# Kernel tuning notes

Hardware: AMD Instinct MI355X
Metric: run time of the kernel (lower is better)

## Reference

```python
import jax, jax.numpy as jnp
import numpy as np

B, S, H, HKV, D = 2, 1024, 32, 8, 128


def _rope_tables(seq_len, head_dim, base=10000.0):
    inv_freq = 1.0 / (base ** (np.arange(0, head_dim, 2, dtype=np.float32) / head_dim))
    freqs = np.arange(seq_len, dtype=np.float32)[:, None] * inv_freq[None, :]  # [S, D/2]
    emb = np.concatenate([freqs, freqs], axis=-1)  # [S, D] (Llama layout)
    return jnp.asarray(np.cos(emb)), jnp.asarray(np.sin(emb))


def setup_inputs() -> dict:
    key = jax.random.key(0)
    kq, kk, kv = jax.random.split(key, 3)
    q = jax.random.normal(kq, (B, S, H, D), dtype=jnp.float32)
    k = jax.random.normal(kk, (B, S, HKV, D), dtype=jnp.float32)
    v = jax.random.normal(kv, (B, S, HKV, D), dtype=jnp.float32)
    cos, sin = _rope_tables(S, D)
    # additive causal mask [B, 1, S, S]: 0 where allowed, large negative where masked
    causal = jnp.tril(jnp.ones((S, S), dtype=bool))
    mask = jnp.where(causal, 0.0, -1e9).astype(jnp.float32)
    attention_mask = jnp.broadcast_to(mask[None, None], (B, 1, S, S))
    softmax_scale = 1.0 / float(np.sqrt(D))
    return {
        "query_states": q, "key_states": k, "value_states": v,
        "cos": cos, "sin": sin, "attention_mask": attention_mask,
        "softmax_scale": softmax_scale,
    }


def _apply_rope(x, cos, sin):
    # x: [B, S, h, D]; cos/sin: [S, D]
    d2 = x.shape[-1] // 2
    rot = jnp.concatenate([-x[..., d2:], x[..., :d2]], axis=-1)  # rotate_half
    return x * cos[None, :, None, :] + rot * sin[None, :, None, :]


def reference(query_states, key_states, value_states, cos, sin, attention_mask, softmax_scale):
    b, s, h, d = query_states.shape
    hkv = key_states.shape[2]
    g = h // hkv  # GQA group size
    q = _apply_rope(query_states, cos, sin)
    k = _apply_rope(key_states, cos, sin)
    qg = q.reshape(b, s, hkv, g, d)
    # scores: [B, Hkv, G, Q, K]
    scores = jnp.einsum('bqhgd,bkhd->bhgqk', qg, k) * softmax_scale
    scores = scores + attention_mask[:, :, None]  # [B,1,Q,K] -> broadcast over (Hkv, G)
    p = jax.nn.softmax(scores, axis=-1)
    out = jnp.einsum('bhgqk,bkhd->bqhgd', p, value_states)
    return out.reshape(b, s, h, d)
```

## Files before the change

### kernel.cpp

```cpp
#include <hip/hip_runtime.h>

#define S_LEN 1024
#define D_DIM 128
#define NH    32
#define NKV   8
#define NB    2

typedef __bf16 bf16x8 __attribute__((ext_vector_type(8)));
typedef float  f32x16 __attribute__((ext_vector_type(16)));
typedef unsigned short u16x8 __attribute__((ext_vector_type(8)));
typedef unsigned int   u32x4 __attribute__((ext_vector_type(4)));

__device__ __forceinline__ unsigned short f2bf(float f) {
    unsigned int u = __float_as_uint(f);
    u += 0x7fffu + ((u >> 16) & 1u);
    return (unsigned short)(u >> 16);
}

__device__ __forceinline__ void gld_lds16(const unsigned short* g, unsigned short* l) {
    __builtin_amdgcn_global_load_lds(
        (const __attribute__((address_space(1))) unsigned int*)(g),
        (__attribute__((address_space(3))) unsigned int*)(l), 16, 0, 0);
}

__global__ __launch_bounds__(256) void prep_kernel(
    const float* __restrict__ q, const float* __restrict__ k,
    const float* __restrict__ v, const float* __restrict__ cosb,
    const float* __restrict__ sinb, const float* __restrict__ scale_ptr,
    unsigned short* __restrict__ Qr, unsigned short* __restrict__ Kr,
    unsigned short* __restrict__ Vt)
{
    const int bx  = blockIdx.x;
    const int tid = threadIdx.x;
    __shared__ __align__(16) unsigned short tile[64][132];
    if (bx < 16384) {
        const float sc = *scale_ptr * 1.44269504088896f;
        int gid = bx * 256 + tid;
        int row = gid >> 6;
        int j   = gid & 63;
        int h  = row & (NH - 1);
        int bs = row >> 5;
        int s  = bs & (S_LEN - 1);
        int b  = bs >> 10;
        const float* qp = q + (size_t)row * D_DIM;
        float x0 = qp[j];
        float x1 = qp[j + 64];
        float c  = cosb[s * D_DIM + j];
        float sn = sinb[s * D_DIM + j];
        size_t orow = ((size_t)(b * NH + h) * S_LEN + s) * D_DIM;
        Qr[orow + j]      = f2bf((x0 * c - x1 * sn) * sc);
        Qr[orow + j + 64] = f2bf((x1 * c + x0 * sn) * sc);
    } else if (bx < 20480) {
        int gid = (bx - 16384) * 256 + tid;
        int row = gid >> 6;
        int j   = gid & 63;
        int hk = row & (NKV - 1);
        int bs = row >> 3;
        int s  = bs & (S_LEN - 1);
        int b  = bs >> 10;
        const float* kp = k + (size_t)row * D_DIM;
        float x0 = kp[j];
        float x1 = kp[j + 64];
        float c  = cosb[s * D_DIM + j];
        float sn = sinb[s * D_DIM + j];
        size_t orow = ((size_t)(b * NKV + hk) * S_LEN + s) * D_DIM;
        Kr[orow + j]      = f2bf(x0 * c - x1 * sn);
        Kr[orow + j + 64] = f2bf(x1 * c + x0 * sn);
    } else {
        int blk   = bx - 20480;
        int stile = blk & 15;
        int hk    = (blk >> 4) & (NKV - 1);
        int b     = blk >> 7;
#pragma unroll
        for (int i = 0; i < 8; i++) {
            int e    = i * 256 + tid;
            int srow = e >> 5;
            int dq   = (e & 31) * 4;
            const float* vp = v + (((size_t)(b * S_LEN + stile * 64 + srow) * NKV + hk) * D_DIM + dq);
            float4 val = *(const float4*)vp;
            tile[srow][dq + 0] = f2bf(val.x);
            tile[srow][dq + 1] = f2bf(val.y);
            tile[srow][dq + 2] = f2bf(val.z);
            tile[srow][dq + 3] = f2bf(val.w);
        }
        __syncthreads();
        size_t head = (size_t)(b * NKV + hk) * D_DIM * S_LEN;
#pragma unroll
        for (int i = 0; i < 4; i++) {
            int g  = i * 256 + tid;
            int d  = g >> 3;
            int c8 = g & 7;
            int s0 = c8 * 8;
            u16x8 pk;
#pragma unroll
            for (int jj = 0; jj < 8; jj++) pk[jj] = tile[s0 + jj][d];
            *(u16x8*)(Vt + head + (size_t)d * S_LEN + stile * 64 + s0) = pk;
        }
    }
}

__global__ __launch_bounds__(256) void attn_kernel(
    const unsigned short* __restrict__ Qr,
    const unsigned short* __restrict__ Kr,
    const unsigned short* __restrict__ Vt,
    float* __restrict__ out)
{
    const int bid  = blockIdx.x;
    const int qt   = 7 - (bid >> 6);
    const int head = bid & 63;
    const int h    = head & 31;
    const int b    = head >> 5;
    const int hk   = h >> 2;

    const int tid  = threadIdx.x;
    const int w    = tid >> 6;
    const int lane = tid & 63;
    const int ln   = lane & 31;
    const int hi   = lane >> 5;

    __shared__ __align__(16) unsigned short Kt[2][64 * 128];
    __shared__ __align__(16) unsigned short Vs[2][128 * 64];

    const int q0 = qt * 128 + w * 32;
    const int qg = q0 + ln;
    const int U  = 2 * qt + 2;

    const unsigned short* khead = Kr + (size_t)(b * NKV + hk) * S_LEN * D_DIM;
    const unsigned short* vhead = Vt + (size_t)(b * NKV + hk) * D_DIM * S_LEN;

    const int krow = lane >> 4;
    const int kcc  = lane & 15;
    const int vrw  = lane >> 3;
    const int vcc  = lane & 7;

    auto stage = [&](int u, int buf) {
        const unsigned short* kt = khead + (size_t)u * 64 * D_DIM;
#pragma unroll
        for (int n = 0; n < 4; n++) {
            int row = w * 16 + n * 4 + krow;
            int cc  = kcc ^ (row & 7);
            gld_lds16(kt + (size_t)row * D_DIM + cc * 8, &Kt[buf][(w * 16 + n * 4) * 128]);
        }
        const unsigned short* vt = vhead + (size_t)u * 64;
#pragma unroll
        for (int n = 0; n < 4; n++) {
            int d  = w * 32 + n * 8 + vrw;
            int cc = vcc ^ (d & 7);
            gld_lds16(vt + (size_t)d * S_LEN + cc * 8, &Vs[buf][(w * 32 + n * 8) * 64]);
        }
    };

    const unsigned short* qrow =
        Qr + ((size_t)(b * NH + h) * S_LEN + qg) * D_DIM + hi * 8;
    bf16x8 qf[8];
#pragma unroll
    for (int dd = 0; dd < 8; dd++)
        qf[dd] = *(const bf16x8*)(qrow + dd * 16);

    f32x16 o[4];
#pragma unroll
    for (int dt = 0; dt < 4; dt++)
#pragma unroll
        for (int r = 0; r < 16; r++) o[dt][r] = 0.f;
    float m_run = -1e30f, lsum = 0.f;

    stage(0, 0);

#pragma unroll 1
    for (int u = 0; u < U; ++u) {
        const int cur = u & 1;
        __syncthreads();
        if (u + 1 < U) stage(u + 1, cur ^ 1);

        if (64 * u <= q0 + 31) {
            const bool act1 = (64 * u + 32 <= q0 + 31);

            f32x16 st[2];
#pragma unroll
            for (int r = 0; r < 16; r++) { st[0][r] = 0.f; st[1][r] = 0.f; }
            __builtin_amdgcn_s_setprio(1);
#pragma unroll
            for (int s = 0; s < 2; s++) {
                if (s == 0 || act1) {
#pragma unroll
                    for (int dd = 0; dd < 8; dd++) {
                        int row = s * 32 + ln;
                        int c   = (2 * dd + hi) ^ (row & 7);
                        bf16x8 kf = *(const bf16x8*)(&Kt[cur][row * 128 + c * 8]);
                        st[s] = __builtin_amdgcn_mfma_f32_32x32x16_bf16(kf, qf[dd], st[s], 0, 0, 0);
                    }
                }
            }
            __builtin_amdgcn_s_setprio(0);

            if (64 * u + 63 > q0) {
#pragma unroll
                for (int s = 0; s < 2; s++)
#pragma unroll
                    for (int r = 0; r < 16; r++) {
                        int kg = 64 * u + 32 * s + (r & 3) + 8 * (r >> 2) + 4 * hi;
                        if (kg > qg) st[s][r] = -1e30f;
                    }
            }

            float mx = -1e30f;
#pragma unroll
            for (int r = 0; r < 16; r++) mx = fmaxf(mx, st[0][r]);
            if (act1) {
#pragma unroll
                for (int r = 0; r < 16; r++) mx = fmaxf(mx, st[1][r]);
            }
            float pm = fmaxf(mx, __shfl_xor(mx, 32));

            if (__any(pm > m_run + 8.f)) {
                float mnew = fmaxf(m_run, pm);
                float ps   = exp2f(m_run - mnew);
                m_run = mnew;
                lsum *= ps;
#pragma unroll
                for (int r = 0; r < 16; r++) {
                    float psr = __shfl(ps, (r & 3) + 8 * (r >> 2) + 4 * hi);
#pragma unroll
                    for (int dt = 0; dt < 4; dt++) o[dt][r] *= psr;
                }
            }
            float ls = 0.f;
#pragma unroll
            for (int r = 0; r < 16; r++) {
                float p = exp2f(st[0][r] - m_run);
                st[0][r] = p; ls += p;
            }
            if (act1) {
#pragma unroll
                for (int r = 0; r < 16; r++) {
                    float p = exp2f(st[1][r] - m_run);
                    st[1][r] = p; ls += p;
                }
            }
            lsum += ls + __shfl_xor(ls, 32);

            const char* vbase = (const char*)&Vs[cur][0];
            __builtin_amdgcn_s_setprio(1);
#pragma unroll
            for (int ks = 0; ks < 4; ks++) {
                if (ks < 2 || act1) {
                    const f32x16& sv = st[ks >> 1];
                    const int g = (ks & 1) * 8;
                    unsigned int d0 = (unsigned)f2bf(sv[g + 0]) | ((unsigned)f2bf(sv[g + 1]) << 16);
                    unsigned int d1 = (unsigned)f2bf(sv[g + 2]) | ((unsigned)f2bf(sv[g + 3]) << 16);
                    unsigned int d2 = (unsigned)f2bf(sv[g + 4]) | ((unsigned)f2bf(sv[g + 5]) << 16);
                    unsigned int d3 = (unsigned)f2bf(sv[g + 6]) | ((unsigned)f2bf(sv[g + 7]) << 16);
                    u32x4 paw = {d0, d1, d2, d3};
                    bf16x8 pa = __builtin_bit_cast(bf16x8, paw);
#pragma unroll
                    for (int dt = 0; dt < 4; dt++) {
                        int d = dt * 32 + ln;
                        const char* vrow = vbase + d * 128;
                        int x = d & 7;
                        uint2 vlo = *(const uint2*)(vrow + (((2 * ks)     ^ x) * 16) + hi * 8);
                        uint2 vhi = *(const uint2*)(vrow + (((2 * ks + 1) ^ x) * 16) + hi * 8);
                        u32x4 vw = {vlo.x, vlo.y, vhi.x, vhi.y};
                        bf16x8 vf = __builtin_bit_cast(bf16x8, vw);
                        o[dt] = __builtin_amdgcn_mfma_f32_32x32x16_bf16(pa, vf, o[dt], 0, 0, 0);
                    }
                }
            }
            __builtin_amdgcn_s_setprio(0);
        }
    }

    float rcp = 1.0f / lsum;
    float* ob = out + ((size_t)(b * S_LEN + q0) * NH + h) * D_DIM;
#pragma unroll
    for (int r = 0; r < 16; r++) {
        int qo = (r & 3) + 8 * (r >> 2) + 4 * hi;
        float invr = __shfl(rcp, qo);
#pragma unroll
        for (int dt = 0; dt < 4; dt++)
            ob[(size_t)qo * NH * D_DIM + dt * 32 + ln] = o[dt][r] * invr;
    }
}

extern "C" void kernel_launch(void* const* d_in, const int* in_sizes, int n_in,
                              void* d_out, int out_size, void* d_ws, size_t ws_size,
                              hipStream_t stream) {
    const float* q    = (const float*)d_in[0];
    const float* k    = (const float*)d_in[1];
    const float* v    = (const float*)d_in[2];
    const float* cosb = (const float*)d_in[3];
    const float* sinb = (const float*)d_in[4];
    const float* scale = (const float*)d_in[6];
    float* out = (float*)d_out;

    unsigned short* Qr = (unsigned short*)d_ws;
    unsigned short* Kr = Qr + (size_t)NB * NH  * S_LEN * D_DIM;
    unsigned short* Vt = Kr + (size_t)NB * NKV * S_LEN * D_DIM;

    prep_kernel<<<20736, 256, 0, stream>>>(q, k, v, cosb, sinb, scale, Qr, Kr, Vt);
    attn_kernel<<<512, 256, 0, stream>>>(Qr, Kr, Vt, out);
}
```

Baseline: 75.92 us.

## Use single-wave attention blocks reading K/V directly from global memory

Replaces the 4-wave workgroup, which staged K and V tiles into LDS with double-buffered async loads, with one-wave workgroups of 32 query rows. Each wave reads K and V straight from global memory through the caches, and a new block-index mapping interleaves heads and balances causal work by pairing long and short query tiles. This removes LDS staging and block barriers and gives the scheduler more independent waves. In exchange, the K/V reuse that LDS provided across the four waves is lost, so more global and L2 traffic is needed, and the V loads become scattered 8-byte reads.

```diff
diff --git a/kernel.cpp b/kernel.cpp
--- a/kernel.cpp
+++ b/kernel.cpp
@@ -15,12 +15,6 @@
     unsigned int u = __float_as_uint(f);
     u += 0x7fffu + ((u >> 16) & 1u);
     return (unsigned short)(u >> 16);
-}
-
-__device__ __forceinline__ void gld_lds16(const unsigned short* g, unsigned short* l) {
-    __builtin_amdgcn_global_load_lds(
-        (const __attribute__((address_space(1))) unsigned int*)(g),
-        (__attribute__((address_space(3))) unsigned int*)(l), 16, 0, 0);
 }
 
 __global__ __launch_bounds__(256) void prep_kernel(
@@ -99,56 +93,35 @@
     }
 }
 
-__global__ __launch_bounds__(256) void attn_kernel(
+__global__ __launch_bounds__(64) void attn_kernel(
     const unsigned short* __restrict__ Qr,
     const unsigned short* __restrict__ Kr,
     const unsigned short* __restrict__ Vt,
     float* __restrict__ out)
 {
-    const int bid  = blockIdx.x;
-    const int qt   = 7 - (bid >> 6);
-    const int head = bid & 63;
-    const int h    = head & 31;
-    const int b    = head >> 5;
-    const int hk   = h >> 2;
-
-    const int tid  = threadIdx.x;
-    const int w    = tid >> 6;
-    const int lane = tid & 63;
+    const int bid = blockIdx.x;
+    const int c   = bid & 255;
+    const int s   = bid >> 8;
+    const int sj  = s & 3;
+    const int hl  = s >> 2;
+    const int cc  = c >> 6;
+    const int m16 = 4 * cc + sj;
+    const int qt  = hl ? (2 * m16) : (31 - 2 * m16);
+    const int head = (c & 7) + 8 * ((c >> 3) & 7);
+    const int h   = head & 31;
+    const int b   = head >> 5;
+    const int hk  = h >> 2;
+
+    const int lane = threadIdx.x;
     const int ln   = lane & 31;
     const int hi   = lane >> 5;
 
-    __shared__ __align__(16) unsigned short Kt[2][64 * 128];
-    __shared__ __align__(16) unsigned short Vs[2][128 * 64];
-
-    const int q0 = qt * 128 + w * 32;
+    const int q0 = qt * 32;
     const int qg = q0 + ln;
-    const int U  = 2 * qt + 2;
+    const int U  = (qt >> 1) + 1;
 
     const unsigned short* khead = Kr + (size_t)(b * NKV + hk) * S_LEN * D_DIM;
     const unsigned short* vhead = Vt + (size_t)(b * NKV + hk) * D_DIM * S_LEN;
-
-    const int krow = lane >> 4;
-    const int kcc  = lane & 15;
-    const int vrw  = lane >> 3;
-    const int vcc  = lane & 7;
-
-    auto stage = [&](int u, int buf) {
-        const unsigned short* kt = khead + (size_t)u * 64 * D_DIM;
-#pragma unroll
-        for (int n = 0; n < 4; n++) {
-            int row = w * 16 + n * 4 + krow;
-            int cc  = kcc ^ (row & 7);
-            gld_lds16(kt + (size_t)row * D_DIM + cc * 8, &Kt[buf][(w * 16 + n * 4) * 128]);
-        }
-        const unsigned short* vt = vhead + (size_t)u * 64;
-#pragma unroll
-        for (int n = 0; n < 4; n++) {
-            int d  = w * 32 + n * 8 + vrw;
-            int cc = vcc ^ (d & 7);
-            gld_lds16(vt + (size_t)d * S_LEN + cc * 8, &Vs[buf][(w * 32 + n * 8) * 64]);
-        }
-    };
 
     const unsigned short* qrow =
         Qr + ((size_t)(b * NH + h) * S_LEN + qg) * D_DIM + hi * 8;
@@ -164,109 +137,99 @@
         for (int r = 0; r < 16; r++) o[dt][r] = 0.f;
     float m_run = -1e30f, lsum = 0.f;
 
-    stage(0, 0);
-
 #pragma unroll 1
     for (int u = 0; u < U; ++u) {
-        const int cur = u & 1;
-        __syncthreads();
-        if (u + 1 < U) stage(u + 1, cur ^ 1);
-
-        if (64 * u <= q0 + 31) {
-            const bool act1 = (64 * u + 32 <= q0 + 31);
-
-            f32x16 st[2];
-#pragma unroll
-            for (int r = 0; r < 16; r++) { st[0][r] = 0.f; st[1][r] = 0.f; }
-            __builtin_amdgcn_s_setprio(1);
-#pragma unroll
-            for (int s = 0; s < 2; s++) {
-                if (s == 0 || act1) {
-#pragma unroll
-                    for (int dd = 0; dd < 8; dd++) {
-                        int row = s * 32 + ln;
-                        int c   = (2 * dd + hi) ^ (row & 7);
-                        bf16x8 kf = *(const bf16x8*)(&Kt[cur][row * 128 + c * 8]);
-                        st[s] = __builtin_amdgcn_mfma_f32_32x32x16_bf16(kf, qf[dd], st[s], 0, 0, 0);
-                    }
+        const unsigned short* kt = khead + (size_t)u * 64 * D_DIM;
+        const unsigned short* vt = vhead + u * 64;
+        const bool act1 = (64 * u + 32 <= q0 + 31);
+
+        f32x16 st[2];
+#pragma unroll
+        for (int r = 0; r < 16; r++) { st[0][r] = 0.f; st[1][r] = 0.f; }
+        __builtin_amdgcn_s_setprio(1);
+#pragma unroll
+        for (int s2 = 0; s2 < 2; s2++) {
+            if (s2 == 0 || act1) {
+                const unsigned short* krow = kt + (size_t)(s2 * 32 + ln) * D_DIM + hi * 8;
+#pragma unroll
+                for (int dd = 0; dd < 8; dd++) {
+                    bf16x8 kf = *(const bf16x8*)(krow + dd * 16);
+                    st[s2] = __builtin_amdgcn_mfma_f32_32x32x16_bf16(kf, qf[dd], st[s2], 0, 0, 0);
                 }
             }
-            __builtin_amdgcn_s_setprio(0);
-
-            if (64 * u + 63 > q0) {
-#pragma unroll
-                for (int s = 0; s < 2; s++)
-#pragma unroll
-                    for (int r = 0; r < 16; r++) {
-                        int kg = 64 * u + 32 * s + (r & 3) + 8 * (r >> 2) + 4 * hi;
-                        if (kg > qg) st[s][r] = -1e30f;
-                    }
-            }
-
-            float mx = -1e30f;
-#pragma unroll
-            for (int r = 0; r < 16; r++) mx = fmaxf(mx, st[0][r]);
-            if (act1) {
-#pragma unroll
-                for (int r = 0; r < 16; r++) mx = fmaxf(mx, st[1][r]);
-            }
-            float pm = fmaxf(mx, __shfl_xor(mx, 32));
-
-            if (__any(pm > m_run + 8.f)) {
-                float mnew = fmaxf(m_run, pm);
-                float ps   = exp2f(m_run - mnew);
-                m_run = mnew;
-                lsum *= ps;
+        }
+        __builtin_amdgcn_s_setprio(0);
+
+        if (64 * u + 63 > q0) {
+#pragma unroll
+            for (int s2 = 0; s2 < 2; s2++)
 #pragma unroll
                 for (int r = 0; r < 16; r++) {
-                    float psr = __shfl(ps, (r & 3) + 8 * (r >> 2) + 4 * hi);
-#pragma unroll
-                    for (int dt = 0; dt < 4; dt++) o[dt][r] *= psr;
+                    int kg = 64 * u + 32 * s2 + (r & 3) + 8 * (r >> 2) + 4 * hi;
+                    if (kg > qg) st[s2][r] = -1e30f;
                 }
-            }
-            float ls = 0.f;
+        }
+
+        float mx = -1e30f;
+#pragma unroll
+        for (int r = 0; r < 16; r++) mx = fmaxf(mx, st[0][r]);
+        if (act1) {
+#pragma unroll
+            for (int r = 0; r < 16; r++) mx = fmaxf(mx, st[1][r]);
+        }
+        float pm = fmaxf(mx, __shfl_xor(mx, 32));
+
+        if (__any(pm > m_run + 8.f)) {
+            float mnew = fmaxf(m_run, pm);
+            float ps   = exp2f(m_run - mnew);
+            m_run = mnew;
+            lsum *= ps;
 #pragma unroll
             for (int r = 0; r < 16; r++) {
-                float p = exp2f(st[0][r] - m_run);
-                st[0][r] = p; ls += p;
-            }
-            if (act1) {
-#pragma unroll
-                for (int r = 0; r < 16; r++) {
-                    float p = exp2f(st[1][r] - m_run);
-                    st[1][r] = p; ls += p;
+                float psr = __shfl(ps, (r & 3) + 8 * (r >> 2) + 4 * hi);
+#pragma unroll
+                for (int dt = 0; dt < 4; dt++) o[dt][r] *= psr;
+            }
+        }
+        float ls = 0.f;
+#pragma unroll
+        for (int r = 0; r < 16; r++) {
+            float p = exp2f(st[0][r] - m_run);
+            st[0][r] = p; ls += p;
+        }
+        if (act1) {
+#pragma unroll
+            for (int r = 0; r < 16; r++) {
+                float p = exp2f(st[1][r] - m_run);
+                st[1][r] = p; ls += p;
+            }
+        }
+        lsum += ls + __shfl_xor(ls, 32);
+
+        __builtin_amdgcn_s_setprio(1);
+#pragma unroll
+        for (int ks = 0; ks < 4; ks++) {
+            if (ks < 2 || act1) {
+                const f32x16& sv = st[ks >> 1];
+                const int g = (ks & 1) * 8;
+                unsigned int d0 = (unsigned)f2bf(sv[g + 0]) | ((unsigned)f2bf(sv[g + 1]) << 16);
+                unsigned int d1 = (unsigned)f2bf(sv[g + 2]) | ((unsigned)f2bf(sv[g + 3]) << 16);
+                unsigned int d2 = (unsigned)f2bf(sv[g + 4]) | ((unsigned)f2bf(sv[g + 5]) << 16);
+                unsigned int d3 = (unsigned)f2bf(sv[g + 6]) | ((unsigned)f2bf(sv[g + 7]) << 16);
+                u32x4 paw = {d0, d1, d2, d3};
+                bf16x8 pa = __builtin_bit_cast(bf16x8, paw);
+#pragma unroll
+                for (int dt = 0; dt < 4; dt++) {
+                    const unsigned short* vrow = vt + (size_t)(dt * 32 + ln) * S_LEN;
+                    uint2 vlo = *(const uint2*)(vrow + ks * 16 + hi * 4);
+                    uint2 vhi2 = *(const uint2*)(vrow + ks * 16 + 8 + hi * 4);
+                    u32x4 vw = {vlo.x, vlo.y, vhi2.x, vhi2.y};
+                    bf16x8 vf = __builtin_bit_cast(bf16x8, vw);
+                    o[dt] = __builtin_amdgcn_mfma_f32_32x32x16_bf16(pa, vf, o[dt], 0, 0, 0);
                 }
             }
-            lsum += ls + __shfl_xor(ls, 32);
-
-            const char* vbase = (const char*)&Vs[cur][0];
-            __builtin_amdgcn_s_setprio(1);
-#pragma unroll
-            for (int ks = 0; ks < 4; ks++) {
-                if (ks < 2 || act1) {
-                    const f32x16& sv = st[ks >> 1];
-                    const int g = (ks & 1) * 8;
-                    unsigned int d0 = (unsigned)f2bf(sv[g + 0]) | ((unsigned)f2bf(sv[g + 1]) << 16);
-                    unsigned int d1 = (unsigned)f2bf(sv[g + 2]) | ((unsigned)f2bf(sv[g + 3]) << 16);
-                    unsigned int d2 = (unsigned)f2bf(sv[g + 4]) | ((unsigned)f2bf(sv[g + 5]) << 16);
-                    unsigned int d3 = (unsigned)f2bf(sv[g + 6]) | ((unsigned)f2bf(sv[g + 7]) << 16);
-                    u32x4 paw = {d0, d1, d2, d3};
-                    bf16x8 pa = __builtin_bit_cast(bf16x8, paw);
-#pragma unroll
-                    for (int dt = 0; dt < 4; dt++) {
-                        int d = dt * 32 + ln;
-                        const char* vrow = vbase + d * 128;
-                        int x = d & 7;
-                        uint2 vlo = *(const uint2*)(vrow + (((2 * ks)     ^ x) * 16) + hi * 8);
-                        uint2 vhi = *(const uint2*)(vrow + (((2 * ks + 1) ^ x) * 16) + hi * 8);
-                        u32x4 vw = {vlo.x, vlo.y, vhi.x, vhi.y};
-                        bf16x8 vf = __builtin_bit_cast(bf16x8, vw);
-                        o[dt] = __builtin_amdgcn_mfma_f32_32x32x16_bf16(pa, vf, o[dt], 0, 0, 0);
-                    }
-                }
-            }
-            __builtin_amdgcn_s_setprio(0);
-        }
+        }
+        __builtin_amdgcn_s_setprio(0);
     }
 
     float rcp = 1.0f / lsum;
@@ -297,5 +260,5 @@
     unsigned short* Vt = Kr + (size_t)NB * NKV * S_LEN * D_DIM;
 
     prep_kernel<<<20736, 256, 0, stream>>>(q, k, v, cosb, sinb, scale, Qr, Kr, Vt);
-    attn_kernel<<<512, 256, 0, stream>>>(Qr, Kr, Vt, out);
-}
+    attn_kernel<<<2048, 64, 0, stream>>>(Qr, Kr, Vt, out);
+}
```

Result: slower. 152.0 us (+100.2%).
